# Kernel tuning notes

Measured on AMD Instinct MI355X. Metric: run time of the kernel, lower is better.

Reference implementation:

```python
import jax, jax.numpy as jnp
import numpy as np

B, S, H = 1, 2048, 4096
NQ, NKV = 32, 8
HD = H // NQ  # 128


def _rope_tables(seq_len, head_dim, base=10000.0):
    inv_freq = 1.0 / (base ** (np.arange(0, head_dim, 2, dtype=np.float32) / head_dim))
    t = np.arange(seq_len, dtype=np.float32)
    freqs = np.outer(t, inv_freq)  # (S, HD/2)
    emb = np.concatenate([freqs, freqs], axis=-1)  # (S, HD)
    return jnp.asarray(np.cos(emb)), jnp.asarray(np.sin(emb))


def setup_inputs() -> dict:
    key = jax.random.key(0)
    ks = jax.random.split(key, 5)
    cos, sin = _rope_tables(S, HD)
    scale = 1.0 / np.sqrt(H)
    return {
        "hidden_states": jax.random.normal(ks[0], (B, S, H), dtype=jnp.float32),
        "cos": cos,
        "sin": sin,
        "wq": jax.random.normal(ks[1], (H, NQ * HD), dtype=jnp.float32) * scale,
        "wk": jax.random.normal(ks[2], (H, NKV * HD), dtype=jnp.float32) * scale,
        "wv": jax.random.normal(ks[3], (H, NKV * HD), dtype=jnp.float32) * scale,
        "wo": jax.random.normal(ks[4], (NQ * HD, H), dtype=jnp.float32) * scale,
    }


def _rotate_half(x):
    x1, x2 = jnp.split(x, 2, axis=-1)
    return jnp.concatenate([-x2, x1], axis=-1)


def reference(hidden_states, cos, sin, wq, wk, wv, wo):
    b, s, _ = hidden_states.shape
    q = (hidden_states @ wq).reshape(b, s, NQ, HD)
    k = (hidden_states @ wk).reshape(b, s, NKV, HD)
    v = (hidden_states @ wv).reshape(b, s, NKV, HD)
    c = cos[None, :, None, :]
    sn = sin[None, :, None, :]
    q = q * c + _rotate_half(q) * sn
    k = k * c + _rotate_half(k) * sn
    groups = NQ // NKV
    # GQA: compute scores per kv-head group without materially repeating K/V beyond einsum
    q = q.reshape(b, s, NKV, groups, HD)
    # scores: (b, kv_head, group, s_q, s_k)
    scores = jnp.einsum("bqhgd,bkhd->bhgqk", q, k) / jnp.sqrt(jnp.asarray(HD, q.dtype))
    causal = jnp.tril(jnp.ones((s, s), dtype=bool))
    scores = jnp.where(causal[None, None, None], scores, jnp.finfo(scores.dtype).min)
    attn = jax.nn.softmax(scores, axis=-1)
    out = jnp.einsum("bhgqk,bkhd->bqhgd", attn, v)  # (b, s, kv_h, g, d)
    out = out.reshape(b, s, NQ * HD)
    return out @ wo
```

## Files before the change

### kernel.cpp

```cpp
#include <hip/hip_runtime.h>
#include <hip/hip_bf16.h>
#include <math.h>

#define S_LEN 2048
#define HDIM  4096
#define NQ_H  32
#define NKV_H 8
#define HD_   128
#define DQ (NQ_H*HD_)
#define DKV (NKV_H*HD_)
#define NFUSE (DQ + 2*DKV)

typedef unsigned short u16;
typedef unsigned int   u32;
typedef __attribute__((ext_vector_type(8))) short short8;
typedef __attribute__((ext_vector_type(4))) float f32x4;

__device__ __forceinline__ u16 bf16_rne(float x) {
    u32 u = __float_as_uint(x);
    u = (u + 0x7FFFu + ((u >> 16) & 1u)) >> 16;
    return (u16)u;
}
__device__ __forceinline__ float bf16_to_f(u16 h) {
    return __uint_as_float(((u32)h) << 16);
}
__device__ __forceinline__ void glds16(const u16* g, u16* l) {
    __builtin_amdgcn_global_load_lds(
        (const __attribute__((address_space(1))) u32*)g,
        (__attribute__((address_space(3))) u32*)l,
        16, 0, 0);
}

__global__ __launch_bounds__(256) void cvt_all(const float* __restrict__ X,
                                               u16* __restrict__ Xb,
                                               const float* __restrict__ wq,
                                               const float* __restrict__ wk,
                                               const float* __restrict__ wv,
                                               u16* __restrict__ WT) {
    __shared__ float tile[32][33];
    const int bid = blockIdx.x;
    if (bid < 4096) {
        int i = (bid * 256 + threadIdx.x) * 8;
        float4 a = *(const float4*)&X[i];
        float4 b = *(const float4*)&X[i + 4];
        u16 h[8];
        h[0] = bf16_rne(a.x); h[1] = bf16_rne(a.y); h[2] = bf16_rne(a.z); h[3] = bf16_rne(a.w);
        h[4] = bf16_rne(b.x); h[5] = bf16_rne(b.y); h[6] = bf16_rne(b.z); h[7] = bf16_rne(b.w);
        *(uint4*)&Xb[i] = *(uint4*)h;
        return;
    }
    const int wid = bid - 4096;
    const int n0g = (wid % 192) * 32;
    const int k0  = (wid / 192) * 32;
    const float* W; int Nsrc, nloc0;
    if (n0g < DQ)            { W = wq; Nsrc = DQ;  nloc0 = n0g; }
    else if (n0g < DQ + DKV) { W = wk; Nsrc = DKV; nloc0 = n0g - DQ; }
    else                     { W = wv; Nsrc = DKV; nloc0 = n0g - DQ - DKV; }
    const int tx = threadIdx.x & 31;
    const int ty = threadIdx.x >> 5;
#pragma unroll
    for (int i = 0; i < 4; ++i)
        tile[ty + 8 * i][tx] = W[(size_t)(k0 + ty + 8 * i) * Nsrc + nloc0 + tx];
    __syncthreads();
#pragma unroll
    for (int i = 0; i < 4; ++i) {
        int r = ty + 8 * i;
        WT[(size_t)(n0g + r) * HDIM + k0 + tx] = bf16_rne(tile[tx][r]);
    }
}

#define AOFFU(par, mh) ((par) * 16384 + (mh) * 8192)
#define BOFFU(par, nh) (32768 + (par) * 16384 + (nh) * 8192)

__global__ __launch_bounds__(512, 2) void gemm_qkv256(const u16* __restrict__ A,
                                                      const u16* __restrict__ BT,
                                                      u16* __restrict__ qb,
                                                      u16* __restrict__ kb,
                                                      u16* __restrict__ vb,
                                                      const float* __restrict__ wo,
                                                      u16* __restrict__ woT) {
    const int K  = HDIM;
    const int NT = K / 64;
    __shared__ u16 smem[65536] __attribute__((aligned(16)));

    const int id = blockIdx.x;
    const int t  = threadIdx.x;

    if (id >= 192) {
        const int b  = id - 192;
        const int n0 = b * 64;
        float* tile = (float*)smem;
        const int r  = t >> 3;
        const int c8 = (t & 7) * 8;
        for (int k0 = 0; k0 < DQ; k0 += 64) {
            float4 x0 = *(const float4*)&wo[(size_t)(k0 + r) * HDIM + n0 + c8];
            float4 x1 = *(const float4*)&wo[(size_t)(k0 + r) * HDIM + n0 + c8 + 4];
            float* tr = &tile[r * 65 + c8];
            tr[0] = x0.x; tr[1] = x0.y; tr[2] = x0.z; tr[3] = x0.w;
            tr[4] = x1.x; tr[5] = x1.y; tr[6] = x1.z; tr[7] = x1.w;
            __syncthreads();
            u16 h[8];
#pragma unroll
            for (int j = 0; j < 8; ++j) h[j] = bf16_rne(tile[(c8 + j) * 65 + r]);
            *(uint4*)&woT[(size_t)(n0 + r) * DQ + k0 + c8] = *(uint4*)h;
            __syncthreads();
        }
        return;
    }

    const int w    = t >> 6;
    const int lane = t & 63;
    const int wm   = w >> 2;
    const int wn   = w & 3;
    const int fr   = lane & 15;
    const int quad = lane >> 4;
    const int m0   = (id / 24) * 256;
    const int n0   = (id % 24) * 256;

    const int lrow = lane >> 3;
    const int lc   = (lane & 7) ^ lrow;
    const u16* const baseA = A  + (size_t)(m0 + w * 16 + lrow) * K + lc * 8;
    const u16* const baseB = BT + (size_t)(n0 + w * 16 + lrow) * K + lc * 8;
    const int wdst = w * 1024;

    const int pc0  = (quad ^ (fr & 7)) * 8;
    const int pc1  = pc0 ^ 32;
    const int aRow = (wm * 64 + fr) * 64;
    const int bRow = (wn * 32 + fr) * 64;

    f32x4 acc[2][2][4][2];
#pragma unroll
    for (int a = 0; a < 2; ++a)
#pragma unroll
        for (int b = 0; b < 2; ++b)
#pragma unroll
            for (int c = 0; c < 4; ++c)
#pragma unroll
                for (int d = 0; d < 2; ++d) acc[a][b][c][d] = (f32x4)0.f;

    short8 ar0[4][2], ar1[4][2], br[2][2];

    auto stA = [&](int off, int tile, int mh) {
        const u16* g = baseA + (size_t)mh * 128 * K + tile * 64;
        glds16(g,                 smem + off + wdst);
        glds16(g + (size_t)8 * K, smem + off + wdst + 512);
    };
    auto stB = [&](int off, int tile, int nh) {
        const u16* g = baseB + (size_t)nh * 128 * K + tile * 64;
        glds16(g,                 smem + off + wdst);
        glds16(g + (size_t)8 * K, smem + off + wdst + 512);
    };
    auto rdA = [&](short8 (&d)[4][2], int off) {
#pragma unroll
        for (int mr = 0; mr < 4; ++mr) {
            d[mr][0] = *(const short8*)&smem[off + aRow + mr * 1024 + pc0];
            d[mr][1] = *(const short8*)&smem[off + aRow + mr * 1024 + pc1];
        }
    };
    auto rdB = [&](short8 (&d)[2][2], int off) {
#pragma unroll
        for (int nc = 0; nc < 2; ++nc) {
            d[nc][0] = *(const short8*)&smem[off + bRow + nc * 1024 + pc0];
            d[nc][1] = *(const short8*)&smem[off + bRow + nc * 1024 + pc1];
        }
    };
    auto mma = [&](short8 (&a)[4][2], short8 (&b)[2][2], f32x4 (&c)[4][2]) {
        __builtin_amdgcn_s_setprio(1);
#pragma unroll
        for (int mr = 0; mr < 4; ++mr)
#pragma unroll
            for (int nc = 0; nc < 2; ++nc) {
                c[mr][nc] = __builtin_amdgcn_mfma_f32_16x16x32_bf16(a[mr][0], b[nc][0], c[mr][nc], 0, 0, 0);
                c[mr][nc] = __builtin_amdgcn_mfma_f32_16x16x32_bf16(a[mr][1], b[nc][1], c[mr][nc], 0, 0, 0);
            }
        __builtin_amdgcn_s_setprio(0);
    };

    stA(AOFFU(0,0), 0, 0);
    stB(BOFFU(0,0), 0, 0);
    stA(AOFFU(0,1), 0, 1);
    stB(BOFFU(0,1), 0, 1);
    stA(AOFFU(1,0), 1, 0);
    stB(BOFFU(1,0), 1, 0);
    stA(AOFFU(1,1), 1, 1);
    asm volatile("s_waitcnt vmcnt(6)" ::: "memory");
    __builtin_amdgcn_s_barrier();

    for (int T = 0; T < NT; T += 2) {
        const int ts2 = (T + 2 < NT) ? T + 2 : NT - 1;
        const int ts3 = (T + 3 < NT) ? T + 3 : NT - 1;
        rdA(ar0, AOFFU(0,0));
        rdB(br,  BOFFU(0,0));
        stB(BOFFU(1,1), T + 1, 1);
        __builtin_amdgcn_s_barrier();
        asm volatile("s_waitcnt lgkmcnt(0)" ::: "memory");
        mma(ar0, br, acc[0][0]);
        __builtin_amdgcn_s_barrier();
        rdA(ar1, AOFFU(0,1));
        stA(AOFFU(0,0), ts2, 0);
        __builtin_amdgcn_s_barrier();
        asm volatile("s_waitcnt lgkmcnt(0)" ::: "memory");
        mma(ar1, br, acc[1][0]);
        __builtin_amdgcn_s_barrier();
        rdB(br, BOFFU(0,1));
        stB(BOFFU(0,0), ts2, 0);
        __builtin_amdgcn_s_barrier();
        asm volatile("s_waitcnt lgkmcnt(0)" ::: "memory");
        mma(ar1, br, acc[1][1]);
        __builtin_amdgcn_s_barrier();
        stA(AOFFU(0,1), ts2, 1);
        __builtin_amdgcn_s_barrier();
        asm volatile("s_waitcnt lgkmcnt(0)" ::: "memory");
        mma(ar0, br, acc[0][1]);
        asm volatile("s_waitcnt vmcnt(6)" ::: "memory");
        __builtin_amdgcn_s_barrier();
        rdA(ar0, AOFFU(1,0));
        rdB(br,  BOFFU(1,0));
        stB(BOFFU(0,1), ts2, 1);
        __builtin_amdgcn_s_barrier();
        asm volatile("s_waitcnt lgkmcnt(0)" ::: "memory");
        mma(ar0, br, acc[0][0]);
        __builtin_amdgcn_s_barrier();
        rdA(ar1, AOFFU(1,1));
        stA(AOFFU(1,0), ts3, 0);
        __builtin_amdgcn_s_barrier();
        asm volatile("s_waitcnt lgkmcnt(0)" ::: "memory");
        mma(ar1, br, acc[1][0]);
        __builtin_amdgcn_s_barrier();
        rdB(br, BOFFU(1,1));
        stB(BOFFU(1,0), ts3, 0);
        __builtin_amdgcn_s_barrier();
        asm volatile("s_waitcnt lgkmcnt(0)" ::: "memory");
        mma(ar1, br, acc[1][1]);
        __builtin_amdgcn_s_barrier();
        stA(AOFFU(1,1), ts3, 1);
        __builtin_amdgcn_s_barrier();
        asm volatile("s_waitcnt lgkmcnt(0)" ::: "memory");
        mma(ar0, br, acc[0][1]);
        asm volatile("s_waitcnt vmcnt(6)" ::: "memory");
        __builtin_amdgcn_s_barrier();
    }

    u16* dst; int stride, nbase;
    if (n0 < DQ)            { dst = qb; stride = DQ;  nbase = n0; }
    else if (n0 < DQ + DKV) { dst = kb; stride = DKV; nbase = n0 - DQ; }
    else                    { dst = vb; stride = DKV; nbase = n0 - DQ - DKV; }

    const int col = lane & 15;
    const int rq  = (lane >> 4) * 4;
#pragma unroll
    for (int mh = 0; mh < 2; ++mh)
#pragma unroll
        for (int nh = 0; nh < 2; ++nh)
#pragma unroll
            for (int mr = 0; mr < 4; ++mr)
#pragma unroll
                for (int nc = 0; nc < 2; ++nc)
#pragma unroll
                    for (int i = 0; i < 4; ++i)
                        dst[(size_t)(m0 + mh * 128 + wm * 64 + mr * 16 + rq + i) * stride
                            + nbase + nh * 128 + wn * 32 + nc * 16 + col] =
                            bf16_rne(acc[mh][nh][mr][nc][i]);
}

__global__ __launch_bounds__(512, 2) void gemm_out256(const u16* __restrict__ A,
                                                      const u16* __restrict__ BT,
                                                      float* __restrict__ C,
                                                      u32* __restrict__ flags) {
    const int LDA = DQ;
    const int NT  = 32;
    __shared__ u16 smem[65536] __attribute__((aligned(16)));

    const int t    = threadIdx.x;
    const int w    = t >> 6;
    const int lane = t & 63;
    const int wm   = w >> 2;
    const int wn   = w & 3;
    const int fr   = lane & 15;
    const int quad = lane >> 4;
    const int m0   = blockIdx.y * 256;
    const int n0   = blockIdx.x * 256;
    const int kz   = blockIdx.z * 2048;
    const int tile_id = blockIdx.y * 16 + blockIdx.x;

    const int lrow = lane >> 3;
    const int lc   = (lane & 7) ^ lrow;
    const u16* const baseA = A  + (size_t)(m0 + w * 16 + lrow) * LDA + kz + lc * 8;
    const u16* const baseB = BT + (size_t)(n0 + w * 16 + lrow) * LDA + kz + lc * 8;
    const int wdst = w * 1024;

    const int pc0  = (quad ^ (fr & 7)) * 8;
    const int pc1  = pc0 ^ 32;
    const int aRow = (wm * 64 + fr) * 64;
    const int bRow = (wn * 32 + fr) * 64;

    f32x4 acc[2][2][4][2];
#pragma unroll
    for (int a = 0; a < 2; ++a)
#pragma unroll
        for (int b = 0; b < 2; ++b)
#pragma unroll
            for (int c = 0; c < 4; ++c)
#pragma unroll
                for (int d = 0; d < 2; ++d) acc[a][b][c][d] = (f32x4)0.f;

    short8 ar0[4][2], ar1[4][2], br[2][2];

    auto stA = [&](int off, int tile, int mh) {
        const u16* g = baseA + (size_t)mh * 128 * LDA + tile * 64;
        glds16(g,                   smem + off + wdst);
        glds16(g + (size_t)8 * LDA, smem + off + wdst + 512);
    };
    auto stB = [&](int off, int tile, int nh) {
        const u16* g = baseB + (size_t)nh * 128 * LDA + tile * 64;
        glds16(g,                   smem + off + wdst);
        glds16(g + (size_t)8 * LDA, smem + off + wdst + 512);
    };
    auto rdA = [&](short8 (&d)[4][2], int off) {
#pragma unroll
        for (int mr = 0; mr < 4; ++mr) {
            d[mr][0] = *(const short8*)&smem[off + aRow + mr * 1024 + pc0];
            d[mr][1] = *(const short8*)&smem[off + aRow + mr * 1024 + pc1];
        }
    };
    auto rdB = [&](short8 (&d)[2][2], int off) {
#pragma unroll
        for (int nc = 0; nc < 2; ++nc) {
            d[nc][0] = *(const short8*)&smem[off + bRow + nc * 1024 + pc0];
            d[nc][1] = *(const short8*)&smem[off + bRow + nc * 1024 + pc1];
        }
    };
    auto mma = [&](short8 (&a)[4][2], short8 (&b)[2][2], f32x4 (&c)[4][2]) {
        __builtin_amdgcn_s_setprio(1);
#pragma unroll
        for (int mr = 0; mr < 4; ++mr)
#pragma unroll
            for (int nc = 0; nc < 2; ++nc) {
                c[mr][nc] = __builtin_amdgcn_mfma_f32_16x16x32_bf16(a[mr][0], b[nc][0], c[mr][nc], 0, 0, 0);
                c[mr][nc] = __builtin_amdgcn_mfma_f32_16x16x32_bf16(a[mr][1], b[nc][1], c[mr][nc], 0, 0, 0);
            }
        __builtin_amdgcn_s_setprio(0);
    };

    stA(AOFFU(0,0), 0, 0);
    stB(BOFFU(0,0), 0, 0);
    stA(AOFFU(0,1), 0, 1);
    stB(BOFFU(0,1), 0, 1);
    stA(AOFFU(1,0), 1, 0);
    stB(BOFFU(1,0), 1, 0);
    stA(AOFFU(1,1), 1, 1);
    asm volatile("s_waitcnt vmcnt(6)" ::: "memory");
    __builtin_amdgcn_s_barrier();

    for (int T = 0; T < NT; T += 2) {
        const int ts2 = (T + 2 < NT) ? T + 2 : NT - 1;
        const int ts3 = (T + 3 < NT) ? T + 3 : NT - 1;
        rdA(ar0, AOFFU(0,0));
        rdB(br,  BOFFU(0,0));
        stB(BOFFU(1,1), T + 1, 1);
        __builtin_amdgcn_s_barrier();
        asm volatile("s_waitcnt lgkmcnt(0)" ::: "memory");
        mma(ar0, br, acc[0][0]);
        __builtin_amdgcn_s_barrier();
        rdA(ar1, AOFFU(0,1));
        stA(AOFFU(0,0), ts2, 0);
        __builtin_amdgcn_s_barrier();
        asm volatile("s_waitcnt lgkmcnt(0)" ::: "memory");
        mma(ar1, br, acc[1][0]);
        __builtin_amdgcn_s_barrier();
        rdB(br, BOFFU(0,1));
        stB(BOFFU(0,0), ts2, 0);
        __builtin_amdgcn_s_barrier();
        asm volatile("s_waitcnt lgkmcnt(0)" ::: "memory");
        mma(ar1, br, acc[1][1]);
        __builtin_amdgcn_s_barrier();
        stA(AOFFU(0,1), ts2, 1);
        __builtin_amdgcn_s_barrier();
        asm volatile("s_waitcnt lgkmcnt(0)" ::: "memory");
        mma(ar0, br, acc[0][1]);
        asm volatile("s_waitcnt vmcnt(6)" ::: "memory");
        __builtin_amdgcn_s_barrier();
        rdA(ar0, AOFFU(1,0));
        rdB(br,  BOFFU(1,0));
        stB(BOFFU(0,1), ts2, 1);
        __builtin_amdgcn_s_barrier();
        asm volatile("s_waitcnt lgkmcnt(0)" ::: "memory");
        mma(ar0, br, acc[0][0]);
        __builtin_amdgcn_s_barrier();
        rdA(ar1, AOFFU(1,1));
        stA(AOFFU(1,0), ts3, 0);
        __builtin_amdgcn_s_barrier();
        asm volatile("s_waitcnt lgkmcnt(0)" ::: "memory");
        mma(ar1, br, acc[1][0]);
        __builtin_amdgcn_s_barrier();
        rdB(br, BOFFU(1,1));
        stB(BOFFU(1,0), ts3, 0);
        __builtin_amdgcn_s_barrier();
        asm volatile("s_waitcnt lgkmcnt(0)" ::: "memory");
        mma(ar1, br, acc[1][1]);
        __builtin_amdgcn_s_barrier();
        stA(AOFFU(1,1), ts3, 1);
        __builtin_amdgcn_s_barrier();
        asm volatile("s_waitcnt lgkmcnt(0)" ::: "memory");
        mma(ar0, br, acc[0][1]);
        asm volatile("s_waitcnt vmcnt(6)" ::: "memory");
        __builtin_amdgcn_s_barrier();
    }

    const int col = lane & 15;
    const int rq  = (lane >> 4) * 4;
    if (blockIdx.z == 0) {
#pragma unroll
        for (int mh = 0; mh < 2; ++mh)
#pragma unroll
            for (int nh = 0; nh < 2; ++nh)
#pragma unroll
                for (int mr = 0; mr < 4; ++mr)
#pragma unroll
                    for (int nc = 0; nc < 2; ++nc)
#pragma unroll
                        for (int i = 0; i < 4; ++i)
                            C[(size_t)(m0 + mh * 128 + wm * 64 + mr * 16 + rq + i) * HDIM
                              + n0 + nh * 128 + wn * 32 + nc * 16 + col] =
                                acc[mh][nh][mr][nc][i];
        __syncthreads();
        if (t == 0)
            __hip_atomic_store(&flags[tile_id], 1u, __ATOMIC_RELEASE, __HIP_MEMORY_SCOPE_AGENT);
    } else {
        if (t == 0) {
            while (__hip_atomic_load(&flags[tile_id], __ATOMIC_ACQUIRE, __HIP_MEMORY_SCOPE_AGENT) == 0u)
                __builtin_amdgcn_s_sleep(2);
        }
        __syncthreads();
#pragma unroll
        for (int mh = 0; mh < 2; ++mh)
#pragma unroll
            for (int nh = 0; nh < 2; ++nh)
#pragma unroll
                for (int mr = 0; mr < 4; ++mr)
#pragma unroll
                    for (int nc = 0; nc < 2; ++nc)
#pragma unroll
                        for (int i = 0; i < 4; ++i) {
                            size_t off = (size_t)(m0 + mh * 128 + wm * 64 + mr * 16 + rq + i) * HDIM
                                         + n0 + nh * 128 + wn * 32 + nc * 16 + col;
                            C[off] += acc[mh][nh][mr][nc][i];
                        }
    }
}

__global__ __launch_bounds__(256) void rope_tv(u16* __restrict__ q, u16* __restrict__ k,
                                               const float* __restrict__ cosT,
                                               const float* __restrict__ sinT,
                                               const u16* __restrict__ V,
                                               u16* __restrict__ Vt) {
    __shared__ u16 tile[64][72];
    const int bid = blockIdx.x;
    const int t = threadIdx.x;
    if (bid < 5120) {
        int idx = bid * 256 + t;
        int d4   = (idx & 15) * 4;
        int rest = idx >> 4;
        int head = rest % (NQ_H + NKV_H);
        int s    = rest / (NQ_H + NKV_H);
        u16* base = (head < NQ_H)
            ? q + ((size_t)s * NQ_H + head) * HD_
            : k + ((size_t)s * NKV_H + (head - NQ_H)) * HD_;
        float4 c  = *(const float4*)&cosT[s * HD_ + d4];
        float4 sn = *(const float4*)&sinT[s * HD_ + d4];
        u16 lo[4], hi[4];
        *(uint2*)lo = *(uint2*)&base[d4];
        *(uint2*)hi = *(uint2*)&base[d4 + 64];
        float cs[4] = {c.x, c.y, c.z, c.w};
        float ss[4] = {sn.x, sn.y, sn.z, sn.w};
        u16 nlo[4], nhi[4];
#pragma unroll
        for (int j = 0; j < 4; ++j) {
            float x1 = bf16_to_f(lo[j]);
            float x2 = bf16_to_f(hi[j]);
            nlo[j] = bf16_rne(x1 * cs[j] - x2 * ss[j]);
            nhi[j] = bf16_rne(x2 * cs[j] + x1 * ss[j]);
        }
        *(uint2*)&base[d4]      = *(uint2*)nlo;
        *(uint2*)&base[d4 + 64] = *(uint2*)nhi;
        return;
    }
    const int b   = bid - 5120;
    const int s0  = (b & 31) * 64;
    const int yy  = b >> 5;
    const int kvh = yy >> 1;
    const int d0  = (yy & 1) * 64;
    const int chunk = t & 7;
    const int row   = t >> 3;
#pragma unroll
    for (int p = 0; p < 2; ++p) {
        int s = row + 32 * p;
        uint4 x = *(const uint4*)&V[(size_t)(s0 + s) * DKV + kvh * HD_ + d0 + chunk * 8];
        *(uint4*)&tile[s][chunk * 8] = x;
    }
    __syncthreads();
#pragma unroll
    for (int p = 0; p < 2; ++p) {
        int d = row + 32 * p;
        u16 tmp[8];
#pragma unroll
        for (int j = 0; j < 8; ++j) tmp[j] = tile[chunk * 8 + j][d];
        *(uint4*)&Vt[(size_t)(kvh * HD_ + d0 + d) * S_LEN + s0 + chunk * 8] = *(uint4*)tmp;
    }
}

#define QSTR 136
#define PSTR 76
__global__ __launch_bounds__(512, 4) void attn_mfma(const u16* __restrict__ Q,
                                                    const u16* __restrict__ K,
                                                    const u16* __restrict__ Vt,
                                                    u16* __restrict__ O) {
    __shared__ u16 smem[26112] __attribute__((aligned(16)));
    u16* sK  = smem;
    u16* sVt = smem + 8192;
    u16* sP  = smem + 16384;
    u16* sQ  = sVt;

    const int id  = blockIdx.x;
    const int h   = id & 31;
    const int qt  = (id < 256) ? (15 - (id >> 5)) : ((id - 256) >> 5);
    const int kvh = h >> 2;
    const int q0  = qt * 128;
    const int t    = threadIdx.x;
    const int w    = t >> 6;
    const int lane = t & 63;
    const int fr   = lane & 15;
    const int quad = lane >> 4;
    const int nkt  = 2 * qt + 2;

    const float K1 = 0.12751744154f;
    const float K2 = 11.5415603267f;

    const int kRow  = t >> 3;
    const int kC    = t & 7;
    const int kLds0 = kRow * 128 + (((2 * kC + 0) ^ (kRow & 7)) * 8);
    const int kLds1 = kRow * 128 + (((2 * kC + 1) ^ (kRow & 7)) * 8);
    const u16* const kGp = K + (size_t)kRow * DKV + (size_t)kvh * HD_ + kC * 16;

    const int vRow  = t >> 2;
    const int vC    = t & 3;
    const int vLds0 = vRow * 64 + (((2 * vC + 0) ^ (vRow & 7)) * 8);
    const int vLds1 = vRow * 64 + (((2 * vC + 1) ^ (vRow & 7)) * 8);
    const u16* const vGp = Vt + ((size_t)kvh * HD_ + vRow) * S_LEN + vC * 16;

    uint4 kr0 = *(const uint4*)(kGp);
    uint4 kr1 = *(const uint4*)(kGp + 8);
    uint4 vr0 = *(const uint4*)(vGp);
    uint4 vr1 = *(const uint4*)(vGp + 8);

    {
        const int col  = t & 15;
        const int row4 = t >> 4;
#pragma unroll
        for (int p = 0; p < 4; ++p) {
            int row = row4 + 32 * p;
            uint4 xv = *(const uint4*)&Q[(size_t)(q0 + row) * DQ + h * HD_ + col * 8];
            *(uint4*)&sQ[row * QSTR + col * 8] = xv;
        }
    }
    __syncthreads();

    short8 aq[4];
#pragma unroll
    for (int ks = 0; ks < 4; ++ks)
        aq[ks] = *(const short8*)&sQ[(16 * w + fr) * QSTR + ks * 32 + quad * 8];

    float lrow[4] = {0.f, 0.f, 0.f, 0.f};
    f32x4 oacc[8];
#pragma unroll
    for (int n8 = 0; n8 < 8; ++n8) oacc[n8] = (f32x4)0.f;

    u16* const sPw   = sP + w * (16 * PSTR);
    const int  qwTop = q0 + 16 * w;

    for (int kt = 0; kt < nkt; ++kt) {
        const int k0 = kt * 64;
        __syncthreads();

        *(uint4*)&sK[kLds0]  = kr0;
        *(uint4*)&sK[kLds1]  = kr1;
        *(uint4*)&sVt[vLds0] = vr0;
        *(uint4*)&sVt[vLds1] = vr1;
        if (kt + 1 < nkt) {
            const u16* kp = kGp + (size_t)(k0 + 64) * DKV;
            kr0 = *(const uint4*)(kp);
            kr1 = *(const uint4*)(kp + 8);
            const u16* vp = vGp + (k0 + 64);
            vr0 = *(const uint4*)(vp);
            vr1 = *(const uint4*)(vp + 8);
        }
        __syncthreads();

        if (k0 <= qwTop + 15) {
            f32x4 sacc[4];
#pragma unroll
            for (int nt = 0; nt < 4; ++nt) sacc[nt] = (f32x4)0.f;
            __builtin_amdgcn_s_setprio(1);
#pragma unroll
            for (int ks = 0; ks < 4; ++ks)
#pragma unroll
                for (int nt = 0; nt < 4; ++nt) {
                    const short8 bk = *(const short8*)
                        &sK[(nt * 16 + fr) * 128 + (((ks * 4 + quad) ^ (fr & 7)) * 8)];
                    sacc[nt] = __builtin_amdgcn_mfma_f32_16x16x32_bf16(aq[ks], bk, sacc[nt], 0, 0, 0);
                }
            __builtin_amdgcn_s_setprio(0);

            if (k0 + 63 > qwTop) {
#pragma unroll
                for (int nt = 0; nt < 4; ++nt) {
                    int key = k0 + nt * 16 + fr;
#pragma unroll
                    for (int i = 0; i < 4; ++i)
                        if (key > qwTop + quad * 4 + i) sacc[nt][i] = -INFINITY;
                }
            }

#pragma unroll
            for (int nt = 0; nt < 4; ++nt)
#pragma unroll
                for (int i = 0; i < 4; ++i) {
                    float p = __builtin_amdgcn_exp2f(fmaf(sacc[nt][i], K1, -K2));
                    lrow[i] += p;
                    sPw[(quad * 4 + i) * PSTR + nt * 16 + fr] = bf16_rne(p);
                }

            __builtin_amdgcn_s_setprio(1);
#pragma unroll
            for (int ks2 = 0; ks2 < 2; ++ks2) {
                const short8 ap = *(const short8*)&sPw[fr * PSTR + ks2 * 32 + quad * 8];
#pragma unroll
                for (int n8 = 0; n8 < 8; ++n8) {
                    const short8 bv = *(const short8*)
                        &sVt[(n8 * 16 + fr) * 64 + (((ks2 * 4 + quad) ^ (fr & 7)) * 8)];
                    oacc[n8] = __builtin_amdgcn_mfma_f32_16x16x32_bf16(ap, bv, oacc[n8], 0, 0, 0);
                }
            }
            __builtin_amdgcn_s_setprio(0);
        }
    }

#pragma unroll
    for (int i = 0; i < 4; ++i) {
        lrow[i] += __shfl_xor(lrow[i], 1);
        lrow[i] += __shfl_xor(lrow[i], 2);
        lrow[i] += __shfl_xor(lrow[i], 4);
        lrow[i] += __shfl_xor(lrow[i], 8);
    }
#pragma unroll
    for (int i = 0; i < 4; ++i) {
        float inv = 1.f / lrow[i];
        size_t base = (size_t)(qwTop + quad * 4 + i) * DQ + h * HD_;
#pragma unroll
        for (int n8 = 0; n8 < 8; ++n8)
            O[base + n8 * 16 + fr] = bf16_rne(oacc[n8][i] * inv);
    }
}

extern "C" void kernel_launch(void* const* d_in, const int* in_sizes, int n_in,
                              void* d_out, int out_size, void* d_ws, size_t ws_size,
                              hipStream_t stream) {
    const float* X    = (const float*)d_in[0];
    const float* cosT = (const float*)d_in[1];
    const float* sinT = (const float*)d_in[2];
    const float* wq   = (const float*)d_in[3];
    const float* wk   = (const float*)d_in[4];
    const float* wv   = (const float*)d_in[5];
    const float* wo   = (const float*)d_in[6];
    float* out = (float*)d_out;

    const size_t SDQ  = (size_t)S_LEN * DQ;
    const size_t SDKV = (size_t)S_LEN * DKV;
    const size_t WQKV = (size_t)HDIM * NFUSE;

    u16* Xb  = (u16*)d_ws;
    u16* qb  = Xb + SDQ;
    u16* kb  = qb + SDQ;
    u16* vb  = kb + SDKV;
    u16* vtb = vb + SDKV;
    u16* aob = vtb + SDKV;
    u16* WT  = aob + SDQ;
    u16* woT = WT + WQKV;

    u32* flags = (u32*)d_ws;

    dim3 blk(256);

    cvt_all<<<dim3(4096 + 24576), blk, 0, stream>>>(X, Xb, wq, wk, wv, WT);

    gemm_qkv256<<<dim3(256), dim3(512), 0, stream>>>(Xb, WT, qb, kb, vb, wo, woT);

    rope_tv<<<dim3(5120 + 512), blk, 0, stream>>>(qb, kb, cosT, sinT, vb, vtb);

    attn_mfma<<<dim3(512), dim3(512), 0, stream>>>(qb, kb, vtb, aob);

    hipMemsetAsync(flags, 0, 128 * sizeof(u32), stream);
    gemm_out256<<<dim3(HDIM / 256, S_LEN / 256, 2), dim3(512), 0, stream>>>(aob, woT, out, flags);
}
```

Baseline: 480.7 us.

## Replace split-K output GEMM with 128x256 tiles over full K

The output projection GEMM drops its two-way split-K scheme, which used flag-based spin-waiting and a read-modify-write second pass plus a memset. It now uses 128x256 output tiles covering the full K dimension. That keeps the grid at 256 blocks but removes the serialized accumulation, the flag sync and the memset launch. The cost is twice as many K iterations per block, with a different smem layout and MFMA schedule per wave.

```diff
diff --git a/kernel.cpp b/kernel.cpp
--- a/kernel.cpp
+++ b/kernel.cpp
@@ -263,13 +263,15 @@
                             bf16_rne(acc[mh][nh][mr][nc][i]);
 }
 
-__global__ __launch_bounds__(512, 2) void gemm_out256(const u16* __restrict__ A,
-                                                      const u16* __restrict__ BT,
-                                                      float* __restrict__ C,
-                                                      u32* __restrict__ flags) {
+#define OAOFF(par)     ((par) * 8192)
+#define OBOFF(par, nh) (16384 + (par) * 16384 + (nh) * 8192)
+
+__global__ __launch_bounds__(512, 2) void gemm_o128(const u16* __restrict__ A,
+                                                    const u16* __restrict__ BT,
+                                                    float* __restrict__ C) {
     const int LDA = DQ;
-    const int NT  = 32;
-    __shared__ u16 smem[65536] __attribute__((aligned(16)));
+    const int NT  = 64;
+    __shared__ u16 smem[49152] __attribute__((aligned(16)));
 
     const int t    = threadIdx.x;
     const int w    = t >> 6;
@@ -278,36 +280,31 @@
     const int wn   = w & 3;
     const int fr   = lane & 15;
     const int quad = lane >> 4;
-    const int m0   = blockIdx.y * 256;
+    const int m0   = blockIdx.y * 128;
     const int n0   = blockIdx.x * 256;
-    const int kz   = blockIdx.z * 2048;
-    const int tile_id = blockIdx.y * 16 + blockIdx.x;
+    const int bh   = wn >> 1;
 
     const int lrow = lane >> 3;
     const int lc   = (lane & 7) ^ lrow;
-    const u16* const baseA = A  + (size_t)(m0 + w * 16 + lrow) * LDA + kz + lc * 8;
-    const u16* const baseB = BT + (size_t)(n0 + w * 16 + lrow) * LDA + kz + lc * 8;
+    const u16* const baseA = A  + (size_t)(m0 + w * 16 + lrow) * LDA + lc * 8;
+    const u16* const baseB = BT + (size_t)(n0 + w * 16 + lrow) * LDA + lc * 8;
     const int wdst = w * 1024;
 
     const int pc0  = (quad ^ (fr & 7)) * 8;
     const int pc1  = pc0 ^ 32;
     const int aRow = (wm * 64 + fr) * 64;
-    const int bRow = (wn * 32 + fr) * 64;
-
-    f32x4 acc[2][2][4][2];
-#pragma unroll
-    for (int a = 0; a < 2; ++a)
-#pragma unroll
-        for (int b = 0; b < 2; ++b)
-#pragma unroll
-            for (int c = 0; c < 4; ++c)
-#pragma unroll
-                for (int d = 0; d < 2; ++d) acc[a][b][c][d] = (f32x4)0.f;
-
-    short8 ar0[4][2], ar1[4][2], br[2][2];
-
-    auto stA = [&](int off, int tile, int mh) {
-        const u16* g = baseA + (size_t)mh * 128 * LDA + tile * 64;
+    const int bRow = ((wn & 1) * 64 + fr) * 64;
+
+    f32x4 acc[4][4];
+#pragma unroll
+    for (int i = 0; i < 4; ++i)
+#pragma unroll
+        for (int j = 0; j < 4; ++j) acc[i][j] = (f32x4)0.f;
+
+    short8 a0[2][2], a1[2][2], b[2][2];
+
+    auto stA = [&](int off, int tile) {
+        const u16* g = baseA + tile * 64;
         glds16(g,                   smem + off + wdst);
         glds16(g + (size_t)8 * LDA, smem + off + wdst + 512);
     };
@@ -316,137 +313,106 @@
         glds16(g,                   smem + off + wdst);
         glds16(g + (size_t)8 * LDA, smem + off + wdst + 512);
     };
-    auto rdA = [&](short8 (&d)[4][2], int off) {
-#pragma unroll
-        for (int mr = 0; mr < 4; ++mr) {
-            d[mr][0] = *(const short8*)&smem[off + aRow + mr * 1024 + pc0];
-            d[mr][1] = *(const short8*)&smem[off + aRow + mr * 1024 + pc1];
-        }
-    };
-    auto rdB = [&](short8 (&d)[2][2], int off) {
-#pragma unroll
-        for (int nc = 0; nc < 2; ++nc) {
-            d[nc][0] = *(const short8*)&smem[off + bRow + nc * 1024 + pc0];
-            d[nc][1] = *(const short8*)&smem[off + bRow + nc * 1024 + pc1];
-        }
-    };
-    auto mma = [&](short8 (&a)[4][2], short8 (&b)[2][2], f32x4 (&c)[4][2]) {
+    auto rdA2 = [&](short8 (&d)[2][2], int off, int qm) {
+#pragma unroll
+        for (int m2 = 0; m2 < 2; ++m2) {
+            d[m2][0] = *(const short8*)&smem[off + aRow + (2 * qm + m2) * 1024 + pc0];
+            d[m2][1] = *(const short8*)&smem[off + aRow + (2 * qm + m2) * 1024 + pc1];
+        }
+    };
+    auto rdB2 = [&](short8 (&d)[2][2], int off, int qn) {
+#pragma unroll
+        for (int n2 = 0; n2 < 2; ++n2) {
+            d[n2][0] = *(const short8*)&smem[off + bRow + (2 * qn + n2) * 1024 + pc0];
+            d[n2][1] = *(const short8*)&smem[off + bRow + (2 * qn + n2) * 1024 + pc1];
+        }
+    };
+    auto mma8 = [&](short8 (&a)[2][2], short8 (&bb)[2][2], int qm, int qn) {
         __builtin_amdgcn_s_setprio(1);
 #pragma unroll
-        for (int mr = 0; mr < 4; ++mr)
-#pragma unroll
-            for (int nc = 0; nc < 2; ++nc) {
-                c[mr][nc] = __builtin_amdgcn_mfma_f32_16x16x32_bf16(a[mr][0], b[nc][0], c[mr][nc], 0, 0, 0);
-                c[mr][nc] = __builtin_amdgcn_mfma_f32_16x16x32_bf16(a[mr][1], b[nc][1], c[mr][nc], 0, 0, 0);
+        for (int m2 = 0; m2 < 2; ++m2)
+#pragma unroll
+            for (int n2 = 0; n2 < 2; ++n2) {
+                acc[2 * qm + m2][2 * qn + n2] = __builtin_amdgcn_mfma_f32_16x16x32_bf16(
+                    a[m2][0], bb[n2][0], acc[2 * qm + m2][2 * qn + n2], 0, 0, 0);
+                acc[2 * qm + m2][2 * qn + n2] = __builtin_amdgcn_mfma_f32_16x16x32_bf16(
+                    a[m2][1], bb[n2][1], acc[2 * qm + m2][2 * qn + n2], 0, 0, 0);
             }
         __builtin_amdgcn_s_setprio(0);
     };
 
-    stA(AOFFU(0,0), 0, 0);
-    stB(BOFFU(0,0), 0, 0);
-    stA(AOFFU(0,1), 0, 1);
-    stB(BOFFU(0,1), 0, 1);
-    stA(AOFFU(1,0), 1, 0);
-    stB(BOFFU(1,0), 1, 0);
-    stA(AOFFU(1,1), 1, 1);
+    stA(OAOFF(0), 0);
+    stB(OBOFF(0,0), 0, 0);
+    stB(OBOFF(0,1), 0, 1);
+    stA(OAOFF(1), 1);
+    stB(OBOFF(1,0), 1, 0);
+    stB(OBOFF(1,1), 1, 1);
     asm volatile("s_waitcnt vmcnt(6)" ::: "memory");
     __builtin_amdgcn_s_barrier();
 
     for (int T = 0; T < NT; T += 2) {
         const int ts2 = (T + 2 < NT) ? T + 2 : NT - 1;
         const int ts3 = (T + 3 < NT) ? T + 3 : NT - 1;
-        rdA(ar0, AOFFU(0,0));
-        rdB(br,  BOFFU(0,0));
-        stB(BOFFU(1,1), T + 1, 1);
-        __builtin_amdgcn_s_barrier();
-        asm volatile("s_waitcnt lgkmcnt(0)" ::: "memory");
-        mma(ar0, br, acc[0][0]);
-        __builtin_amdgcn_s_barrier();
-        rdA(ar1, AOFFU(0,1));
-        stA(AOFFU(0,0), ts2, 0);
-        __builtin_amdgcn_s_barrier();
-        asm volatile("s_waitcnt lgkmcnt(0)" ::: "memory");
-        mma(ar1, br, acc[1][0]);
-        __builtin_amdgcn_s_barrier();
-        rdB(br, BOFFU(0,1));
-        stB(BOFFU(0,0), ts2, 0);
-        __builtin_amdgcn_s_barrier();
-        asm volatile("s_waitcnt lgkmcnt(0)" ::: "memory");
-        mma(ar1, br, acc[1][1]);
-        __builtin_amdgcn_s_barrier();
-        stA(AOFFU(0,1), ts2, 1);
-        __builtin_amdgcn_s_barrier();
-        asm volatile("s_waitcnt lgkmcnt(0)" ::: "memory");
-        mma(ar0, br, acc[0][1]);
+        rdA2(a0, OAOFF(0), 0);
+        rdB2(b,  OBOFF(0, bh), 0);
+        __builtin_amdgcn_s_barrier();
+        asm volatile("s_waitcnt lgkmcnt(0)" ::: "memory");
+        mma8(a0, b, 0, 0);
+        __builtin_amdgcn_s_barrier();
+        rdA2(a1, OAOFF(0), 1);
+        __builtin_amdgcn_s_barrier();
+        asm volatile("s_waitcnt lgkmcnt(0)" ::: "memory");
+        mma8(a1, b, 1, 0);
+        __builtin_amdgcn_s_barrier();
+        rdB2(b, OBOFF(0, bh), 1);
+        stA(OAOFF(0), ts2);
+        __builtin_amdgcn_s_barrier();
+        asm volatile("s_waitcnt lgkmcnt(0)" ::: "memory");
+        mma8(a1, b, 1, 1);
+        __builtin_amdgcn_s_barrier();
+        stB(OBOFF(0,0), ts2, 0);
+        stB(OBOFF(0,1), ts2, 1);
+        __builtin_amdgcn_s_barrier();
+        asm volatile("s_waitcnt lgkmcnt(0)" ::: "memory");
+        mma8(a0, b, 0, 1);
         asm volatile("s_waitcnt vmcnt(6)" ::: "memory");
         __builtin_amdgcn_s_barrier();
-        rdA(ar0, AOFFU(1,0));
-        rdB(br,  BOFFU(1,0));
-        stB(BOFFU(0,1), ts2, 1);
-        __builtin_amdgcn_s_barrier();
-        asm volatile("s_waitcnt lgkmcnt(0)" ::: "memory");
-        mma(ar0, br, acc[0][0]);
-        __builtin_amdgcn_s_barrier();
-        rdA(ar1, AOFFU(1,1));
-        stA(AOFFU(1,0), ts3, 0);
-        __builtin_amdgcn_s_barrier();
-        asm volatile("s_waitcnt lgkmcnt(0)" ::: "memory");
-        mma(ar1, br, acc[1][0]);
-        __builtin_amdgcn_s_barrier();
-        rdB(br, BOFFU(1,1));
-        stB(BOFFU(1,0), ts3, 0);
-        __builtin_amdgcn_s_barrier();
-        asm volatile("s_waitcnt lgkmcnt(0)" ::: "memory");
-        mma(ar1, br, acc[1][1]);
-        __builtin_amdgcn_s_barrier();
-        stA(AOFFU(1,1), ts3, 1);
-        __builtin_amdgcn_s_barrier();
-        asm volatile("s_waitcnt lgkmcnt(0)" ::: "memory");
-        mma(ar0, br, acc[0][1]);
+        rdA2(a0, OAOFF(1), 0);
+        rdB2(b,  OBOFF(1, bh), 0);
+        __builtin_amdgcn_s_barrier();
+        asm volatile("s_waitcnt lgkmcnt(0)" ::: "memory");
+        mma8(a0, b, 0, 0);
+        __builtin_amdgcn_s_barrier();
+        rdA2(a1, OAOFF(1), 1);
+        __builtin_amdgcn_s_barrier();
+        asm volatile("s_waitcnt lgkmcnt(0)" ::: "memory");
+        mma8(a1, b, 1, 0);
+        __builtin_amdgcn_s_barrier();
+        rdB2(b, OBOFF(1, bh), 1);
+        stA(OAOFF(1), ts3);
+        __builtin_amdgcn_s_barrier();
+        asm volatile("s_waitcnt lgkmcnt(0)" ::: "memory");
+        mma8(a1, b, 1, 1);
+        __builtin_amdgcn_s_barrier();
+        stB(OBOFF(1,0), ts3, 0);
+        stB(OBOFF(1,1), ts3, 1);
+        __builtin_amdgcn_s_barrier();
+        asm volatile("s_waitcnt lgkmcnt(0)" ::: "memory");
+        mma8(a0, b, 0, 1);
         asm volatile("s_waitcnt vmcnt(6)" ::: "memory");
         __builtin_amdgcn_s_barrier();
     }
 
     const int col = lane & 15;
     const int rq  = (lane >> 4) * 4;
-    if (blockIdx.z == 0) {
-#pragma unroll
-        for (int mh = 0; mh < 2; ++mh)
-#pragma unroll
-            for (int nh = 0; nh < 2; ++nh)
-#pragma unroll
-                for (int mr = 0; mr < 4; ++mr)
-#pragma unroll
-                    for (int nc = 0; nc < 2; ++nc)
-#pragma unroll
-                        for (int i = 0; i < 4; ++i)
-                            C[(size_t)(m0 + mh * 128 + wm * 64 + mr * 16 + rq + i) * HDIM
-                              + n0 + nh * 128 + wn * 32 + nc * 16 + col] =
-                                acc[mh][nh][mr][nc][i];
-        __syncthreads();
-        if (t == 0)
-            __hip_atomic_store(&flags[tile_id], 1u, __ATOMIC_RELEASE, __HIP_MEMORY_SCOPE_AGENT);
-    } else {
-        if (t == 0) {
-            while (__hip_atomic_load(&flags[tile_id], __ATOMIC_ACQUIRE, __HIP_MEMORY_SCOPE_AGENT) == 0u)
-                __builtin_amdgcn_s_sleep(2);
-        }
-        __syncthreads();
-#pragma unroll
-        for (int mh = 0; mh < 2; ++mh)
-#pragma unroll
-            for (int nh = 0; nh < 2; ++nh)
-#pragma unroll
-                for (int mr = 0; mr < 4; ++mr)
-#pragma unroll
-                    for (int nc = 0; nc < 2; ++nc)
-#pragma unroll
-                        for (int i = 0; i < 4; ++i) {
-                            size_t off = (size_t)(m0 + mh * 128 + wm * 64 + mr * 16 + rq + i) * HDIM
-                                         + n0 + nh * 128 + wn * 32 + nc * 16 + col;
-                            C[off] += acc[mh][nh][mr][nc][i];
-                        }
-    }
+#pragma unroll
+    for (int mr = 0; mr < 4; ++mr)
+#pragma unroll
+        for (int nc = 0; nc < 4; ++nc)
+#pragma unroll
+            for (int i = 0; i < 4; ++i)
+                C[(size_t)(m0 + wm * 64 + mr * 16 + rq + i) * HDIM
+                  + n0 + wn * 64 + nc * 16 + col] = acc[mr][nc][i];
 }
 
 __global__ __launch_bounds__(256) void rope_tv(u16* __restrict__ q, u16* __restrict__ k,
@@ -687,8 +653,6 @@
     u16* WT  = aob + SDQ;
     u16* woT = WT + WQKV;
 
-    u32* flags = (u32*)d_ws;
-
     dim3 blk(256);
 
     cvt_all<<<dim3(4096 + 24576), blk, 0, stream>>>(X, Xb, wq, wk, wv, WT);
@@ -699,6 +663,5 @@
 
     attn_mfma<<<dim3(512), dim3(512), 0, stream>>>(qb, kb, vtb, aob);
 
-    hipMemsetAsync(flags, 0, 128 * sizeof(u32), stream);
-    gemm_out256<<<dim3(HDIM / 256, S_LEN / 256, 2), dim3(512), 0, stream>>>(aob, woT, out, flags);
-}
+    gemm_o128<<<dim3(HDIM / 256, S_LEN / 128), dim3(512), 0, stream>>>(aob, woT, out);
+}
```

New measurement: 434.0 us. 1.11x faster.
